# Performance work log

Measured on AMD Instinct MI355X. Metric: run time of the kernel, lower is better.

## Reference

```python
import jax, jax.numpy as jnp
import numpy as np

B, S, D, H = 2, 2048, 1024, 16
DH = D // H  # depth per head = 64


def setup_inputs() -> dict:
    key = jax.random.key(0)
    ks = jax.random.split(key, 5)
    sc = 0.02
    return {
        "x": jax.random.normal(ks[0], (B, S, D), dtype=jnp.float32),
        "Wq": jax.random.normal(ks[1], (D, D), dtype=jnp.float32) * sc,
        "bq": jnp.zeros((D,), dtype=jnp.float32),
        "Wk": jax.random.normal(ks[2], (D, D), dtype=jnp.float32) * sc,
        "bk": jnp.zeros((D,), dtype=jnp.float32),
        "Wv": jax.random.normal(ks[3], (D, D), dtype=jnp.float32) * sc,
        "bv": jnp.zeros((D,), dtype=jnp.float32),
        "Wo": jax.random.normal(ks[4], (D, D), dtype=jnp.float32) * sc,
        "bo": jnp.zeros((D,), dtype=jnp.float32),
    }


def _split_heads(t):
    # [B,S,D] -> [B,H,S,DH]
    return t.reshape(B, S, H, DH).transpose(0, 2, 1, 3)


def reference(x, Wq, bq, Wk, bk, Wv, bv, Wo, bo):
    q = _split_heads(x @ Wq + bq)
    k = _split_heads(x @ Wk + bk)
    v = _split_heads(x @ Wv + bv)
    scale = 1.0 / jnp.sqrt(jnp.float32(DH))
    logits = jnp.einsum("bhqd,bhkd->bhqk", q, k) * scale  # [B,H,S,S]
    attn = jax.nn.softmax(logits, axis=-1)
    ctx = jnp.einsum("bhqk,bhkd->bhqd", attn, v)
    ctx = ctx.transpose(0, 2, 1, 3).reshape(B, S, D)
    # dropout is identity at inference
    return ctx @ Wo + bo
```

## Files before the change

### kernel.cpp

```cpp
#include <hip/hip_runtime.h>
#include <hip/hip_bf16.h>

#define S_LEN   2048
#define D_MODEL 1024
#define NHEAD   16
#define DHEAD   64
#define M_ROWS  4096
#define BHEADS  32
#define MEG     1048576

typedef __attribute__((ext_vector_type(8)))  short short8;
typedef __attribute__((ext_vector_type(4)))  float f32x4;
typedef __attribute__((ext_vector_type(16))) float f32x16;
typedef __attribute__((ext_vector_type(4)))  unsigned short us4;

extern "C" __device__ float __ocml_native_exp2_f32(float);

__device__ __forceinline__ unsigned short f2b(float f) {
    unsigned int u = __builtin_bit_cast(unsigned int, f);
    return (unsigned short)((u + 0x7FFFu + ((u >> 16) & 1u)) >> 16);
}

__device__ __forceinline__ unsigned int pk2b(float lo, float hi) {
    unsigned int u0 = __builtin_bit_cast(unsigned int, lo) + 0x8000u;
    unsigned int u1 = __builtin_bit_cast(unsigned int, hi) + 0x8000u;
    return __builtin_amdgcn_perm(u1, u0, 0x07060302u);
}

__device__ __forceinline__ float b2f(unsigned short b) {
    return __builtin_bit_cast(float, (unsigned int)b << 16);
}

#define GLOAD16(gp, lp) __builtin_amdgcn_global_load_lds(                     \
        (const __attribute__((address_space(1))) void*)(gp),                  \
        (__attribute__((address_space(3))) void*)(lp), 16, 0, 0)

#define STAGE_OFS(lane) ((((lane) & 3) ^ (((lane) >> 3) & 3)) * 8)

__global__ __launch_bounds__(256) void prep(
    const float* __restrict__ x, unsigned short* __restrict__ xb,
    const float* __restrict__ Wq, const float* __restrict__ Wk,
    const float* __restrict__ Wv, const float* __restrict__ Wo,
    unsigned short* __restrict__ Wqt, unsigned short* __restrict__ Wkt,
    unsigned short* __restrict__ Wvt, unsigned short* __restrict__ Wot)
{
    const int z = blockIdx.z;
    const int tx = threadIdx.x, ty = threadIdx.y;
    if (z == 4) {
        const int blk = blockIdx.y * 32 + blockIdx.x;
        const int base = (blk * 256 + ty * 32 + tx) * 4;
        #pragma unroll
        for (int r = 0; r < 4; ++r) {
            const int i = base + r * (M_ROWS * D_MODEL / 4);
            const float4 v = *(const float4*)&x[i];
            us4 o;
            o.x = f2b(v.x); o.y = f2b(v.y); o.z = f2b(v.z); o.w = f2b(v.w);
            *(us4*)&xb[i] = o;
        }
        return;
    }
    __shared__ float tile[32][33];
    const float* W = z == 0 ? Wq : (z == 1 ? Wk : (z == 2 ? Wv : Wo));
    unsigned short* Wt = z == 0 ? Wqt : (z == 1 ? Wkt : (z == 2 ? Wvt : Wot));
    const int n0 = blockIdx.x * 32, k0 = blockIdx.y * 32;
    #pragma unroll
    for (int i = 0; i < 4; ++i)
        tile[ty + i * 8][tx] = W[(size_t)(k0 + ty + i * 8) * D_MODEL + n0 + tx];
    __syncthreads();
    #pragma unroll
    for (int i = 0; i < 4; ++i)
        Wt[(size_t)(n0 + ty + i * 8) * D_MODEL + k0 + tx] = f2b(tile[tx][ty + i * 8]);
}

__global__ __launch_bounds__(256) void gemm_qkv(
    const unsigned short* __restrict__ xb,
    const unsigned short* __restrict__ Wqt, const unsigned short* __restrict__ Wkt,
    const unsigned short* __restrict__ Wvt,
    const float* __restrict__ bq, const float* __restrict__ bk,
    const float* __restrict__ bv,
    unsigned short* __restrict__ Qb, unsigned short* __restrict__ Kb,
    unsigned short* __restrict__ Vt)
{
    __shared__ unsigned short As[2][128][32];
    __shared__ unsigned short Bs[2][128][32];

    const int z = blockIdx.z;
    const unsigned short* Wt = z == 0 ? Wqt : (z == 1 ? Wkt : Wvt);
    const float* bias = z == 0 ? bq : (z == 1 ? bk : bv);

    const int t = threadIdx.x, lane = t & 63, w = t >> 6;
    const int wm = w >> 1, wn = w & 1;
    const int bm = blockIdx.y * 128, bn = blockIdx.x * 128;
    const int lr = lane >> 2, lc = STAGE_OFS(lane);
    const int lm = lane & 15, quad = lane >> 4;
    const int qo = (quad ^ ((lm >> 1) & 3)) * 8;

    f32x4 acc[4][4] = {};

    #pragma unroll
    for (int i = 0; i < 2; ++i) {
        const int c = 2 * w + i;
        GLOAD16(xb + (size_t)(bm + c * 16 + lr) * D_MODEL + lc, &As[0][c * 16][0]);
        GLOAD16(Wt + (size_t)(bn + c * 16 + lr) * D_MODEL + lc, &Bs[0][c * 16][0]);
    }
    __syncthreads();

    for (int it = 0; it < 32; ++it) {
        const int cur = it & 1;
        if (it + 1 < 32) {
            const int kt = (it + 1) * 32;
            #pragma unroll
            for (int i = 0; i < 2; ++i) {
                const int c = 2 * w + i;
                GLOAD16(xb + (size_t)(bm + c * 16 + lr) * D_MODEL + kt + lc,
                        &As[cur ^ 1][c * 16][0]);
                GLOAD16(Wt + (size_t)(bn + c * 16 + lr) * D_MODEL + kt + lc,
                        &Bs[cur ^ 1][c * 16][0]);
            }
        }

        short8 af[4], bfr[4];
        #pragma unroll
        for (int mi = 0; mi < 4; ++mi)
            af[mi] = *(const short8*)&As[cur][wm * 64 + mi * 16 + lm][qo];
        #pragma unroll
        for (int ni = 0; ni < 4; ++ni)
            bfr[ni] = *(const short8*)&Bs[cur][wn * 64 + ni * 16 + lm][qo];
        #pragma unroll
        for (int mi = 0; mi < 4; ++mi)
            #pragma unroll
            for (int ni = 0; ni < 4; ++ni)
                acc[mi][ni] = __builtin_amdgcn_mfma_f32_16x16x32_bf16(
                    af[mi], bfr[ni], acc[mi][ni], 0, 0, 0);

        __syncthreads();
    }

    float bb[4];
    #pragma unroll
    for (int ni = 0; ni < 4; ++ni)
        bb[ni] = bias[bn + wn * 64 + ni * 16 + lm];
    const float scale = (z == 0) ? 0.18033688011112042f : 1.0f;

    if (z < 2) {
        unsigned short* Out = (z == 0) ? Qb : Kb;
        #pragma unroll
        for (int mi = 0; mi < 4; ++mi)
            #pragma unroll
            for (int r = 0; r < 4; ++r) {
                const int row = bm + wm * 64 + mi * 16 + quad * 4 + r;
                const int b = row >> 11, s = row & 2047;
                #pragma unroll
                for (int ni = 0; ni < 4; ++ni) {
                    const int col = bn + wn * 64 + ni * 16 + lm;
                    const int h = col >> 6, d = col & 63;
                    Out[(((size_t)(b * NHEAD + h)) * S_LEN + s) * DHEAD + d] =
                        f2b((acc[mi][ni][r] + bb[ni]) * scale);
                }
            }
    } else {
        #pragma unroll
        for (int mi = 0; mi < 4; ++mi) {
            const int row0 = bm + wm * 64 + mi * 16 + quad * 4;
            const int b = row0 >> 11, s0 = row0 & 2047;
            #pragma unroll
            for (int ni = 0; ni < 4; ++ni) {
                const int col = bn + wn * 64 + ni * 16 + lm;
                const int h = col >> 6, d = col & 63;
                us4 pk;
                pk.x = f2b(acc[mi][ni][0] + bb[ni]);
                pk.y = f2b(acc[mi][ni][1] + bb[ni]);
                pk.z = f2b(acc[mi][ni][2] + bb[ni]);
                pk.w = f2b(acc[mi][ni][3] + bb[ni]);
                *(us4*)&Vt[(((size_t)(b * NHEAD + h)) * DHEAD + d) * S_LEN + s0] = pk;
            }
        }
    }
}

__global__ __launch_bounds__(256) void gemm_out(
    const unsigned short* __restrict__ Ab, const unsigned short* __restrict__ Wot,
    const float* __restrict__ bo, float* __restrict__ out)
{
    __shared__ unsigned short As[2][64][32];
    __shared__ unsigned short Bs[2][128][32];

    const int t = threadIdx.x, lane = t & 63, w = t >> 6;
    const int wm = w & 1, wn = w >> 1;
    const int bm = blockIdx.y * 64, bn = blockIdx.x * 128;
    const int lr = lane >> 2, lc = STAGE_OFS(lane);
    const int lm = lane & 15, quad = lane >> 4;
    const int qo = (quad ^ ((lm >> 1) & 3)) * 8;

    f32x4 acc[2][4] = {};

    GLOAD16(Ab + (size_t)(bm + w * 16 + lr) * D_MODEL + lc, &As[0][w * 16][0]);
    #pragma unroll
    for (int i = 0; i < 2; ++i)
        GLOAD16(Wot + (size_t)(bn + w * 32 + i * 16 + lr) * D_MODEL + lc,
                &Bs[0][w * 32 + i * 16][0]);
    __syncthreads();

    for (int it = 0; it < 32; ++it) {
        const int cur = it & 1;
        if (it + 1 < 32) {
            const int kt = (it + 1) * 32;
            GLOAD16(Ab + (size_t)(bm + w * 16 + lr) * D_MODEL + kt + lc,
                    &As[cur ^ 1][w * 16][0]);
            #pragma unroll
            for (int i = 0; i < 2; ++i)
                GLOAD16(Wot + (size_t)(bn + w * 32 + i * 16 + lr) * D_MODEL + kt + lc,
                        &Bs[cur ^ 1][w * 32 + i * 16][0]);
        }

        short8 af[2], bfr[4];
        #pragma unroll
        for (int mi = 0; mi < 2; ++mi)
            af[mi] = *(const short8*)&As[cur][wm * 32 + mi * 16 + lm][qo];
        #pragma unroll
        for (int ni = 0; ni < 4; ++ni)
            bfr[ni] = *(const short8*)&Bs[cur][wn * 64 + ni * 16 + lm][qo];
        #pragma unroll
        for (int mi = 0; mi < 2; ++mi)
            #pragma unroll
            for (int ni = 0; ni < 4; ++ni)
                acc[mi][ni] = __builtin_amdgcn_mfma_f32_16x16x32_bf16(
                    af[mi], bfr[ni], acc[mi][ni], 0, 0, 0);

        __syncthreads();
    }

    float bb[4];
    #pragma unroll
    for (int ni = 0; ni < 4; ++ni)
        bb[ni] = bo[bn + wn * 64 + ni * 16 + lm];

    #pragma unroll
    for (int mi = 0; mi < 2; ++mi)
        #pragma unroll
        for (int r = 0; r < 4; ++r) {
            const int row = bm + wm * 32 + mi * 16 + quad * 4 + r;
            #pragma unroll
            for (int ni = 0; ni < 4; ++ni) {
                const int col = bn + wn * 64 + ni * 16 + lm;
                out[(size_t)row * D_MODEL + col] = acc[mi][ni][r] + bb[ni];
            }
        }
}

__global__ __launch_bounds__(256, 4) void attn_mfma(
    const unsigned short* __restrict__ Q, const unsigned short* __restrict__ K,
    const unsigned short* __restrict__ V,
    unsigned short* __restrict__ Opart, float* __restrict__ Lpart)
{
    __shared__ __align__(16) unsigned char QPraw[18432];
    unsigned short (*Qs)[128][32] = (unsigned short (*)[128][32])QPraw;
    unsigned int   (*Ps)[32][36]  = (unsigned int   (*)[32][36])QPraw;
    __shared__ unsigned short Ks[2][64][32];
    __shared__ unsigned short Vs[2][64][32];

    const int t = threadIdx.x, lane = t & 63, w = t >> 6;
    const int q5 = lane & 31, hi = lane >> 5;
    const int lr = lane >> 2, lcs = STAGE_OFS(lane);
    const int q0 = blockIdx.x * 128, bh = blockIdx.y, split = blockIdx.z;
    const int k_base = split * (S_LEN / 2);
    const int sw = (q5 >> 1) & 3;
    int sbo[4];
    #pragma unroll
    for (int sb = 0; sb < 4; ++sb) sbo[sb] = (sb ^ sw) * 8;

    const unsigned short* Qh = Q + (size_t)bh * (S_LEN * DHEAD);
    const unsigned short* Kh = K + (size_t)bh * (S_LEN * DHEAD);
    const unsigned short* Vh = V + (size_t)bh * (DHEAD * S_LEN);

    #pragma unroll
    for (int i = 0; i < 2; ++i)
        #pragma unroll
        for (int c = 0; c < 2; ++c)
            GLOAD16(Qh + (size_t)(q0 + w * 32 + c * 16 + lr) * DHEAD + i * 32 + lcs,
                    &Qs[i][w * 32 + c * 16][0]);
    __syncthreads();

    short8 qf[4];
    #pragma unroll
    for (int c = 0; c < 4; ++c)
        qf[c] = *(const short8*)&Qs[c >> 1][w * 32 + q5][sbo[(c & 1) * 2 + hi]];

    f32x16 acc[2] = {};
    float2 l2a = {0.f, 0.f}, l2b = {0.f, 0.f};

    for (int it = 0; it < 16; ++it) {
        const int kt = k_base + it * 64;
        __syncthreads();
        #pragma unroll
        for (int i = 0; i < 2; ++i) {
            GLOAD16(Kh + (size_t)(kt + w * 16 + lr) * DHEAD + i * 32 + lcs,
                    &Ks[i][w * 16][0]);
            GLOAD16(Vh + (size_t)(w * 16 + lr) * S_LEN + kt + i * 32 + lcs,
                    &Vs[i][w * 16][0]);
        }
        __syncthreads();

        f32x16 sf[2] = {};
        #pragma unroll
        for (int c = 0; c < 4; ++c) {
            #pragma unroll
            for (int mt = 0; mt < 2; ++mt) {
                const short8 kf =
                    *(const short8*)&Ks[c >> 1][mt * 32 + q5][sbo[(c & 1) * 2 + hi]];
                sf[mt] = __builtin_amdgcn_mfma_f32_32x32x16_bf16(kf, qf[c], sf[mt], 0, 0, 0);
            }
        }

        #pragma unroll
        for (int mt = 0; mt < 2; ++mt)
            #pragma unroll
            for (int g = 0; g < 4; ++g) {
                const float p0 = __ocml_native_exp2_f32(sf[mt][g * 4 + 0]);
                const float p1 = __ocml_native_exp2_f32(sf[mt][g * 4 + 1]);
                const float p2 = __ocml_native_exp2_f32(sf[mt][g * 4 + 2]);
                const float p3 = __ocml_native_exp2_f32(sf[mt][g * 4 + 3]);
                l2a.x += p0; l2a.y += p1;
                l2b.x += p2; l2b.y += p3;
                uint2 pk;
                pk.x = pk2b(p0, p1);
                pk.y = pk2b(p2, p3);
                *(uint2*)&Ps[w][q5][mt * 16 + g * 4 + hi * 2] = pk;
            }

        #pragma unroll
        for (int c = 0; c < 4; ++c) {
            const short8 pf = *(const short8*)&Ps[w][q5][c * 8 + hi * 4];
            #pragma unroll
            for (int nt = 0; nt < 2; ++nt) {
                const short8 vf =
                    *(const short8*)&Vs[c >> 1][nt * 32 + q5][sbo[(c & 1) * 2 + hi]];
                acc[nt] = __builtin_amdgcn_mfma_f32_32x32x16_bf16(pf, vf, acc[nt], 0, 0, 0);
            }
        }
    }

    float l_acc = (l2a.x + l2a.y) + (l2b.x + l2b.y);
    l_acc += __shfl_xor(l_acc, 32);
    const size_t pbase = ((size_t)(split * BHEADS + bh)) * S_LEN;
    if (hi == 0)
        Lpart[pbase + q0 + w * 32 + q5] = l_acc;
    #pragma unroll
    for (int reg = 0; reg < 16; ++reg) {
        const int row = (reg & 3) + 8 * (reg >> 2) + 4 * hi;
        const size_t obase = (pbase + q0 + w * 32 + row) * DHEAD;
        Opart[obase + q5]      = f2b(acc[0][reg]);
        Opart[obase + 32 + q5] = f2b(acc[1][reg]);
    }
}

__global__ __launch_bounds__(256) void attn_reduce(
    const unsigned short* __restrict__ Op, const float* __restrict__ Lp,
    unsigned short* __restrict__ Cx)
{
    const int idx = blockIdx.x * 256 + threadIdx.x;
    const int gi = idx * 4;
    const int bh = gi >> 17;
    const int rem = gi & (S_LEN * DHEAD - 1);
    const int s = rem >> 6, d = rem & 63;
    const size_t o0 = (size_t)bh * (S_LEN * DHEAD) + rem;
    const size_t o1 = o0 + (size_t)BHEADS * S_LEN * DHEAD;
    const us4 a = *(const us4*)&Op[o0];
    const us4 c = *(const us4*)&Op[o1];
    const float inv = 1.f / (Lp[bh * S_LEN + s] + Lp[BHEADS * S_LEN + bh * S_LEN + s]);
    us4 o;
    o.x = f2b((b2f(a.x) + b2f(c.x)) * inv);
    o.y = f2b((b2f(a.y) + b2f(c.y)) * inv);
    o.z = f2b((b2f(a.z) + b2f(c.z)) * inv);
    o.w = f2b((b2f(a.w) + b2f(c.w)) * inv);
    const int b = bh >> 4, h = bh & 15;
    *(us4*)&Cx[((size_t)(b * S_LEN + s)) * D_MODEL + h * DHEAD + d] = o;
}

extern "C" void kernel_launch(void* const* d_in, const int* in_sizes, int n_in,
                              void* d_out, int out_size, void* d_ws, size_t ws_size,
                              hipStream_t stream)
{
    const float* x  = (const float*)d_in[0];
    const float* Wq = (const float*)d_in[1];
    const float* bq = (const float*)d_in[2];
    const float* Wk = (const float*)d_in[3];
    const float* bk = (const float*)d_in[4];
    const float* Wv = (const float*)d_in[5];
    const float* bv = (const float*)d_in[6];
    const float* Wo = (const float*)d_in[7];
    const float* bo = (const float*)d_in[8];
    float* out = (float*)d_out;

    unsigned short* base = (unsigned short*)d_ws;
    unsigned short* Wot   = base;
    unsigned short* Qb    = base + 1 * MEG;
    unsigned short* Kb    = base + 5 * MEG;
    unsigned short* Vt    = base + 9 * MEG;
    unsigned short* Cxb   = base + 13 * MEG;
    unsigned short* xb    = base + 17 * MEG;
    unsigned short* Wqt   = base + 21 * MEG;
    unsigned short* Wkt   = base + 22 * MEG;
    unsigned short* Wvt   = base + 23 * MEG;
    unsigned short* Opart = xb;
    float*          Lpart = (float*)(base + 25 * MEG);

    prep<<<dim3(32, 32, 5), dim3(32, 8), 0, stream>>>(
        x, xb, Wq, Wk, Wv, Wo, Wqt, Wkt, Wvt, Wot);

    gemm_qkv<<<dim3(D_MODEL / 128, M_ROWS / 128, 3), dim3(256), 0, stream>>>(
        xb, Wqt, Wkt, Wvt, bq, bk, bv, Qb, Kb, Vt);

    attn_mfma<<<dim3(S_LEN / 128, BHEADS, 2), dim3(256), 0, stream>>>(
        Qb, Kb, Vt, Opart, Lpart);

    attn_reduce<<<dim3(BHEADS * S_LEN * DHEAD / 1024), dim3(256), 0, stream>>>(
        Opart, Lpart, Cxb);

    gemm_out<<<dim3(D_MODEL / 128, M_ROWS / 64), dim3(256), 0, stream>>>(
        Cxb, Wot, bo, out);
}
```

Measured before the change: 205.8 us.

## Fuse split-KV reduction into output GEMM and use 32x32 MFMA in QKV GEMM

The separate attn_reduce kernel is removed. gemm_out now reads both split partial outputs and their row sums directly, normalises and packs them to bf16 in registers, and writes them into the swizzled A tile in shared memory, with the next tile's loads overlapped with the current MFMAs. This drops one launch and a full round trip of the context tensor through global memory. Each output-GEMM block now redoes the reduction for its rows, once per column block, so partial loads are repeated eight times. The QKV GEMM also switches from 16x16x32 to 32x32x16 MFMA tiles, changing fragment loads and the epilogue store pattern.

```diff
diff --git a/kernel.cpp b/kernel.cpp
--- a/kernel.cpp
+++ b/kernel.cpp
@@ -8,6 +8,7 @@
 #define M_ROWS  4096
 #define BHEADS  32
 #define MEG     1048576
+#define SPLIT_STRIDE 4194304
 
 typedef __attribute__((ext_vector_type(8)))  short short8;
 typedef __attribute__((ext_vector_type(4)))  float f32x4;
@@ -92,10 +93,13 @@
     const int wm = w >> 1, wn = w & 1;
     const int bm = blockIdx.y * 128, bn = blockIdx.x * 128;
     const int lr = lane >> 2, lc = STAGE_OFS(lane);
-    const int lm = lane & 15, quad = lane >> 4;
-    const int qo = (quad ^ ((lm >> 1) & 3)) * 8;
-
-    f32x4 acc[4][4] = {};
+    const int q5 = lane & 31, hi = lane >> 5;
+    const int sw = (q5 >> 1) & 3;
+    int sbo[4];
+    #pragma unroll
+    for (int sb = 0; sb < 4; ++sb) sbo[sb] = (sb ^ sw) * 8;
+
+    f32x16 acc[2][2] = {};
 
     #pragma unroll
     for (int i = 0; i < 2; ++i) {
@@ -119,67 +123,77 @@
             }
         }
 
-        short8 af[4], bfr[4];
-        #pragma unroll
-        for (int mi = 0; mi < 4; ++mi)
-            af[mi] = *(const short8*)&As[cur][wm * 64 + mi * 16 + lm][qo];
-        #pragma unroll
-        for (int ni = 0; ni < 4; ++ni)
-            bfr[ni] = *(const short8*)&Bs[cur][wn * 64 + ni * 16 + lm][qo];
-        #pragma unroll
-        for (int mi = 0; mi < 4; ++mi)
-            #pragma unroll
-            for (int ni = 0; ni < 4; ++ni)
-                acc[mi][ni] = __builtin_amdgcn_mfma_f32_16x16x32_bf16(
-                    af[mi], bfr[ni], acc[mi][ni], 0, 0, 0);
+        short8 af[2][2], bf2[2][2];
+        #pragma unroll
+        for (int mt = 0; mt < 2; ++mt)
+            #pragma unroll
+            for (int c = 0; c < 2; ++c)
+                af[mt][c] = *(const short8*)&As[cur][wm * 64 + mt * 32 + q5][sbo[c * 2 + hi]];
+        #pragma unroll
+        for (int nt = 0; nt < 2; ++nt)
+            #pragma unroll
+            for (int c = 0; c < 2; ++c)
+                bf2[nt][c] = *(const short8*)&Bs[cur][wn * 64 + nt * 32 + q5][sbo[c * 2 + hi]];
+        #pragma unroll
+        for (int c = 0; c < 2; ++c)
+            #pragma unroll
+            for (int mt = 0; mt < 2; ++mt)
+                #pragma unroll
+                for (int nt = 0; nt < 2; ++nt)
+                    acc[mt][nt] = __builtin_amdgcn_mfma_f32_32x32x16_bf16(
+                        af[mt][c], bf2[nt][c], acc[mt][nt], 0, 0, 0);
 
         __syncthreads();
     }
 
-    float bb[4];
-    #pragma unroll
-    for (int ni = 0; ni < 4; ++ni)
-        bb[ni] = bias[bn + wn * 64 + ni * 16 + lm];
+    float bb2[2];
+    #pragma unroll
+    for (int nt = 0; nt < 2; ++nt)
+        bb2[nt] = bias[bn + wn * 64 + nt * 32 + q5];
     const float scale = (z == 0) ? 0.18033688011112042f : 1.0f;
 
     if (z < 2) {
         unsigned short* Out = (z == 0) ? Qb : Kb;
         #pragma unroll
-        for (int mi = 0; mi < 4; ++mi)
-            #pragma unroll
-            for (int r = 0; r < 4; ++r) {
-                const int row = bm + wm * 64 + mi * 16 + quad * 4 + r;
-                const int b = row >> 11, s = row & 2047;
+        for (int mt = 0; mt < 2; ++mt)
+            #pragma unroll
+            for (int nt = 0; nt < 2; ++nt) {
+                const int col = bn + wn * 64 + nt * 32 + q5;
+                const int h = col >> 6, d = col & 63;
                 #pragma unroll
-                for (int ni = 0; ni < 4; ++ni) {
-                    const int col = bn + wn * 64 + ni * 16 + lm;
-                    const int h = col >> 6, d = col & 63;
+                for (int reg = 0; reg < 16; ++reg) {
+                    const int row = bm + wm * 64 + mt * 32 +
+                                    (reg & 3) + 8 * (reg >> 2) + 4 * hi;
+                    const int b = row >> 11, s = row & 2047;
                     Out[(((size_t)(b * NHEAD + h)) * S_LEN + s) * DHEAD + d] =
-                        f2b((acc[mi][ni][r] + bb[ni]) * scale);
+                        f2b((acc[mt][nt][reg] + bb2[nt]) * scale);
                 }
             }
     } else {
         #pragma unroll
-        for (int mi = 0; mi < 4; ++mi) {
-            const int row0 = bm + wm * 64 + mi * 16 + quad * 4;
-            const int b = row0 >> 11, s0 = row0 & 2047;
-            #pragma unroll
-            for (int ni = 0; ni < 4; ++ni) {
-                const int col = bn + wn * 64 + ni * 16 + lm;
+        for (int mt = 0; mt < 2; ++mt)
+            #pragma unroll
+            for (int nt = 0; nt < 2; ++nt) {
+                const int col = bn + wn * 64 + nt * 32 + q5;
                 const int h = col >> 6, d = col & 63;
-                us4 pk;
-                pk.x = f2b(acc[mi][ni][0] + bb[ni]);
-                pk.y = f2b(acc[mi][ni][1] + bb[ni]);
-                pk.z = f2b(acc[mi][ni][2] + bb[ni]);
-                pk.w = f2b(acc[mi][ni][3] + bb[ni]);
-                *(us4*)&Vt[(((size_t)(b * NHEAD + h)) * DHEAD + d) * S_LEN + s0] = pk;
-            }
-        }
+                #pragma unroll
+                for (int g = 0; g < 4; ++g) {
+                    const int row0 = bm + wm * 64 + mt * 32 + 8 * g + 4 * hi;
+                    const int b = row0 >> 11, s0 = row0 & 2047;
+                    us4 pk;
+                    pk.x = f2b(acc[mt][nt][4 * g + 0] + bb2[nt]);
+                    pk.y = f2b(acc[mt][nt][4 * g + 1] + bb2[nt]);
+                    pk.z = f2b(acc[mt][nt][4 * g + 2] + bb2[nt]);
+                    pk.w = f2b(acc[mt][nt][4 * g + 3] + bb2[nt]);
+                    *(us4*)&Vt[(((size_t)(b * NHEAD + h)) * DHEAD + d) * S_LEN + s0] = pk;
+                }
+            }
     }
 }
 
 __global__ __launch_bounds__(256) void gemm_out(
-    const unsigned short* __restrict__ Ab, const unsigned short* __restrict__ Wot,
+    const unsigned short* __restrict__ Op, const float* __restrict__ Lp,
+    const unsigned short* __restrict__ Wot,
     const float* __restrict__ bo, float* __restrict__ out)
 {
     __shared__ unsigned short As[2][64][32];
@@ -192,9 +206,30 @@
     const int lm = lane & 15, quad = lane >> 4;
     const int qo = (quad ^ ((lm >> 1) & 3)) * 8;
 
+    const int ar  = t >> 2;
+    const int asb = t & 3;
+    const int aps = (asb ^ ((ar >> 1) & 3)) * 8;
+    const int arow = bm + ar;
+    const int ab = arow >> 11, as_ = arow & 2047;
+
     f32x4 acc[2][4] = {};
 
-    GLOAD16(Ab + (size_t)(bm + w * 16 + lr) * D_MODEL + lc, &As[0][w * 16][0]);
+    {
+        const int d0 = asb * 8;
+        const int li = (ab * NHEAD) * S_LEN + as_;
+        const size_t ob = (size_t)li * DHEAD + d0;
+        const us4 pa0 = *(const us4*)&Op[ob];
+        const us4 pa1 = *(const us4*)&Op[ob + 4];
+        const us4 pb0 = *(const us4*)&Op[ob + SPLIT_STRIDE];
+        const us4 pb1 = *(const us4*)&Op[ob + SPLIT_STRIDE + 4];
+        const float inv = 1.f / (Lp[li] + Lp[BHEADS * S_LEN + li]);
+        uint4 r;
+        r.x = pk2b((b2f(pa0.x) + b2f(pb0.x)) * inv, (b2f(pa0.y) + b2f(pb0.y)) * inv);
+        r.y = pk2b((b2f(pa0.z) + b2f(pb0.z)) * inv, (b2f(pa0.w) + b2f(pb0.w)) * inv);
+        r.z = pk2b((b2f(pa1.x) + b2f(pb1.x)) * inv, (b2f(pa1.y) + b2f(pb1.y)) * inv);
+        r.w = pk2b((b2f(pa1.z) + b2f(pb1.z)) * inv, (b2f(pa1.w) + b2f(pb1.w)) * inv);
+        *(short8*)&As[0][ar][aps] = __builtin_bit_cast(short8, r);
+    }
     #pragma unroll
     for (int i = 0; i < 2; ++i)
         GLOAD16(Wot + (size_t)(bn + w * 32 + i * 16 + lr) * D_MODEL + lc,
@@ -203,14 +238,24 @@
 
     for (int it = 0; it < 32; ++it) {
         const int cur = it & 1;
-        if (it + 1 < 32) {
+        us4 pa0, pa1, pb0, pb1;
+        float inv = 0.f;
+        const bool pf = (it + 1 < 32);
+        if (pf) {
             const int kt = (it + 1) * 32;
-            GLOAD16(Ab + (size_t)(bm + w * 16 + lr) * D_MODEL + kt + lc,
-                    &As[cur ^ 1][w * 16][0]);
             #pragma unroll
             for (int i = 0; i < 2; ++i)
                 GLOAD16(Wot + (size_t)(bn + w * 32 + i * 16 + lr) * D_MODEL + kt + lc,
                         &Bs[cur ^ 1][w * 32 + i * 16][0]);
+            const int h = kt >> 6;
+            const int d0 = (kt & 63) + asb * 8;
+            const int li = (ab * NHEAD + h) * S_LEN + as_;
+            const size_t ob = (size_t)li * DHEAD + d0;
+            pa0 = *(const us4*)&Op[ob];
+            pa1 = *(const us4*)&Op[ob + 4];
+            pb0 = *(const us4*)&Op[ob + SPLIT_STRIDE];
+            pb1 = *(const us4*)&Op[ob + SPLIT_STRIDE + 4];
+            inv = 1.f / (Lp[li] + Lp[BHEADS * S_LEN + li]);
         }
 
         short8 af[2], bfr[4];
@@ -227,6 +272,14 @@
                 acc[mi][ni] = __builtin_amdgcn_mfma_f32_16x16x32_bf16(
                     af[mi], bfr[ni], acc[mi][ni], 0, 0, 0);
 
+        if (pf) {
+            uint4 r;
+            r.x = pk2b((b2f(pa0.x) + b2f(pb0.x)) * inv, (b2f(pa0.y) + b2f(pb0.y)) * inv);
+            r.y = pk2b((b2f(pa0.z) + b2f(pb0.z)) * inv, (b2f(pa0.w) + b2f(pb0.w)) * inv);
+            r.z = pk2b((b2f(pa1.x) + b2f(pb1.x)) * inv, (b2f(pa1.y) + b2f(pb1.y)) * inv);
+            r.w = pk2b((b2f(pa1.z) + b2f(pb1.z)) * inv, (b2f(pa1.w) + b2f(pb1.w)) * inv);
+            *(short8*)&As[cur ^ 1][ar][aps] = __builtin_bit_cast(short8, r);
+        }
         __syncthreads();
     }
 
@@ -352,29 +405,6 @@
         Opart[obase + q5]      = f2b(acc[0][reg]);
         Opart[obase + 32 + q5] = f2b(acc[1][reg]);
     }
-}
-
-__global__ __launch_bounds__(256) void attn_reduce(
-    const unsigned short* __restrict__ Op, const float* __restrict__ Lp,
-    unsigned short* __restrict__ Cx)
-{
-    const int idx = blockIdx.x * 256 + threadIdx.x;
-    const int gi = idx * 4;
-    const int bh = gi >> 17;
-    const int rem = gi & (S_LEN * DHEAD - 1);
-    const int s = rem >> 6, d = rem & 63;
-    const size_t o0 = (size_t)bh * (S_LEN * DHEAD) + rem;
-    const size_t o1 = o0 + (size_t)BHEADS * S_LEN * DHEAD;
-    const us4 a = *(const us4*)&Op[o0];
-    const us4 c = *(const us4*)&Op[o1];
-    const float inv = 1.f / (Lp[bh * S_LEN + s] + Lp[BHEADS * S_LEN + bh * S_LEN + s]);
-    us4 o;
-    o.x = f2b((b2f(a.x) + b2f(c.x)) * inv);
-    o.y = f2b((b2f(a.y) + b2f(c.y)) * inv);
-    o.z = f2b((b2f(a.z) + b2f(c.z)) * inv);
-    o.w = f2b((b2f(a.w) + b2f(c.w)) * inv);
-    const int b = bh >> 4, h = bh & 15;
-    *(us4*)&Cx[((size_t)(b * S_LEN + s)) * D_MODEL + h * DHEAD + d] = o;
 }
 
 extern "C" void kernel_launch(void* const* d_in, const int* in_sizes, int n_in,
@@ -397,7 +427,6 @@
     unsigned short* Qb    = base + 1 * MEG;
     unsigned short* Kb    = base + 5 * MEG;
     unsigned short* Vt    = base + 9 * MEG;
-    unsigned short* Cxb   = base + 13 * MEG;
     unsigned short* xb    = base + 17 * MEG;
     unsigned short* Wqt   = base + 21 * MEG;
     unsigned short* Wkt   = base + 22 * MEG;
@@ -414,9 +443,6 @@
     attn_mfma<<<dim3(S_LEN / 128, BHEADS, 2), dim3(256), 0, stream>>>(
         Qb, Kb, Vt, Opart, Lpart);
 
-    attn_reduce<<<dim3(BHEADS * S_LEN * DHEAD / 1024), dim3(256), 0, stream>>>(
-        Opart, Lpart, Cxb);
-
     gemm_out<<<dim3(D_MODEL / 128, M_ROWS / 64), dim3(256), 0, stream>>>(
-        Cxb, Wot, bo, out);
-}
+        Opart, Lpart, Wot, bo, out);
+}
```

After: 207.6 us. About the same (+0.9%).
